# Optimization experiments

Hardware: AMD Instinct MI355X
Metric: run time of the kernel (lower is better)

Reference implementation:

```python
import jax, jax.numpy as jnp
import numpy as np

B, T, C, F = 8, 8, 1024, 4
N = T * C  # 8192 neurons
GUMBEL_KEY = 42  # fixed key standing in for torch's gumbel noise


def setup_inputs() -> dict:
    key = jax.random.key(0)
    kx, kw = jax.random.split(key)
    x = jax.random.normal(kx, (B * N, F), dtype=jnp.float32)
    # stacked ParameterList: weights[t] has shape [B, C, C]
    weights = jax.random.normal(kw, (T, B, C, C), dtype=jnp.float32)
    # cell type of each neuron; equal group sizes (1024 per type), interleaved
    cell_type_indices = (jnp.arange(N) % T).astype(jnp.int32)
    return {"x": x, "weights": weights, "cell_type_indices": cell_type_indices}


def reference(x, weights, cell_type_indices):
    n_types, bsz, cnt, _ = weights.shape
    nf = x.shape[-1]
    xr = x.reshape(bsz, -1, nf)  # [B, N, F]
    # per-type neuron indices, ascending within each type (pandas .index order);
    # stable argsort over types groups them contiguously -> [T, C]
    idx = jnp.argsort(cell_type_indices, stable=True).reshape(n_types, cnt)
    # gumbel_softmax(logits, tau=1, dim=1): softmax over the row axis (axis=2 here)
    g = jax.random.gumbel(jax.random.key(GUMBEL_KEY), weights.shape, weights.dtype)
    soft = jax.nn.softmax(weights + g, axis=2)  # [T, B, C, C]
    gathered = xr[:, idx]  # [B, T, C, F] per-group gather
    # grouped weighted matmul: out[t] = soft[t] @ gathered[:, t]
    res = jnp.einsum('tbij,btjf->btif', soft, gathered)  # [B, T, C, F]
    out = jnp.zeros_like(xr).at[:, idx].set(res)  # scatter back
    return out.reshape(-1, nf)
```

## Files before the change

### kernel.cpp

```cpp
#include <hip/hip_runtime.h>
#include <hip/hip_bf16.h>
#include <stdint.h>


__device__ __forceinline__ uint32_t rotl32(uint32_t x, uint32_t r) {
  return (x << r) | (x >> (32u - r));
}

__device__ __forceinline__ void threefry2x32(uint32_t c0, uint32_t c1,
                                             uint32_t& o0, uint32_t& o1) {
  const uint32_t k0 = 0u, k1 = 42u, k2 = 0x1BD11BDAu ^ 0u ^ 42u;
  uint32_t x0 = c0 + k0;
  uint32_t x1 = c1 + k1;
#define TF_R(r) { x0 += x1; x1 = rotl32(x1, r); x1 ^= x0; }
  TF_R(13) TF_R(15) TF_R(26) TF_R(6)
  x0 += k1; x1 += k2 + 1u;
  TF_R(17) TF_R(29) TF_R(16) TF_R(24)
  x0 += k2; x1 += k0 + 2u;
  TF_R(13) TF_R(15) TF_R(26) TF_R(6)
  x0 += k0; x1 += k1 + 3u;
  TF_R(17) TF_R(29) TF_R(16) TF_R(24)
  x0 += k1; x1 += k2 + 4u;
  TF_R(13) TF_R(15) TF_R(26) TF_R(6)
  x0 += k2; x1 += k0 + 5u;
#undef TF_R
  o0 = x0; o1 = x1;
}

__device__ __forceinline__ float gumbel_of(uint32_t e) {
  uint32_t o0, o1;
  threefry2x32(0u, e, o0, o1);
  uint32_t bits = o0 ^ o1;
  float f = __uint_as_float((bits >> 9) | 0x3f800000u) - 1.0f;
  f = fmaxf(f, 1.1754943508222875e-38f);
  return -__logf(-__logf(f));
}

template <int MODE>
__global__ __launch_bounds__(256) void pass1_kernel(
    const float* __restrict__ w, float* __restrict__ s, void* __restrict__ pout) {
  const int blk = blockIdx.x;
  const int ic  = blk & 63;
  const int tb  = blk >> 6;
  const int tid = threadIdx.x;
  const int i0  = ic * 16;

  const float4* w4 = (const float4*)w;
  const int base = tb * (1024 * 256) + i0 * 256 + tid;
  const uint32_t e_base = ((uint32_t)tb * 1024u + (uint32_t)i0) * 1024u + 4u * tid;

  float s0 = 0.f, s1 = 0.f, s2 = 0.f, s3 = 0.f;
  for (int r = 0; r < 16; ++r) {
    float4 wv = w4[base + r * 256];
    uint32_t e = e_base + (uint32_t)r * 1024u;
    float p0 = __expf(wv.x + gumbel_of(e + 0u));
    float p1 = __expf(wv.y + gumbel_of(e + 1u));
    float p2 = __expf(wv.z + gumbel_of(e + 2u));
    float p3 = __expf(wv.w + gumbel_of(e + 3u));
    s0 += p0; s1 += p1; s2 += p2; s3 += p3;
    if (MODE == 0) {
      ((float4*)pout)[base + r * 256] = make_float4(p0, p1, p2, p3);
    } else if (MODE == 1) {
      uint32_t b0 = (uint32_t)__bfloat16_as_ushort(__float2bfloat16(p0));
      uint32_t b1 = (uint32_t)__bfloat16_as_ushort(__float2bfloat16(p1));
      uint32_t b2 = (uint32_t)__bfloat16_as_ushort(__float2bfloat16(p2));
      uint32_t b3 = (uint32_t)__bfloat16_as_ushort(__float2bfloat16(p3));
      uint2 pk = make_uint2(b0 | (b1 << 16), b2 | (b3 << 16));
      ((uint2*)pout)[base + r * 256] = pk;
    }
  }
  float* sp = s + tb * 1024 + 4 * tid;
  atomicAdd(sp + 0, s0);
  atomicAdd(sp + 1, s1);
  atomicAdd(sp + 2, s2);
  atomicAdd(sp + 3, s3);
}

__device__ __forceinline__ void stage_y(const float* __restrict__ x,
                                        const float* __restrict__ s,
                                        int tb, int t, int b, int tid,
                                        float4* ylds) {
  const float4* x4 = (const float4*)x;
  for (int q = 0; q < 4; ++q) {
    int j = tid + 256 * q;
    float4 xv = x4[b * 8192 + t + 8 * j];
    float inv = 1.0f / s[tb * 1024 + j];
    int slot = (j & ~7) | ((j + (j >> 3)) & 7);
    ylds[slot] = make_float4(xv.x * inv, xv.y * inv, xv.z * inv, xv.w * inv);
  }
}

__device__ __forceinline__ void reduce_store(float a0, float a1, float a2, float a3,
                                             int lane, int b, int t, int i,
                                             float* __restrict__ out) {
#pragma unroll
  for (int mask = 32; mask >= 1; mask >>= 1) {
    a0 += __shfl_xor(a0, mask, 64);
    a1 += __shfl_xor(a1, mask, 64);
    a2 += __shfl_xor(a2, mask, 64);
    a3 += __shfl_xor(a3, mask, 64);
  }
  if (lane == 0) {
    ((float4*)out)[b * 8192 + t + 8 * i] = make_float4(a0, a1, a2, a3);
  }
}

__global__ __launch_bounds__(256) void pass2f_kernel(
    const float* __restrict__ p, const float* __restrict__ x,
    const float* __restrict__ s, float* __restrict__ out) {
  __shared__ float4 ylds[1024];
  const int blk = blockIdx.x;
  const int ig  = blk & 63;
  const int tb  = blk >> 6;
  const int t   = tb >> 3;
  const int b   = tb & 7;
  const int tid = threadIdx.x;

  stage_y(x, s, tb, t, b, tid, ylds);
  __syncthreads();

  const int wave = tid >> 6;
  const int lane = tid & 63;
  const float4* p4 = (const float4*)p;

  for (int rr = 0; rr < 4; ++rr) {
    const int i = ig * 16 + wave * 4 + rr;
    const int wbase = (tb * 1024 + i) * 256;
    float a0 = 0.f, a1 = 0.f, a2 = 0.f, a3 = 0.f;
#pragma unroll
    for (int m = 0; m < 4; ++m) {
      float4 pv = p4[wbase + lane + 64 * m];
      int jb = 4 * lane + 256 * m;
      float pr[4] = {pv.x, pv.y, pv.z, pv.w};
#pragma unroll
      for (int r = 0; r < 4; ++r) {
        int j = jb + r;
        int slot = (j & ~7) | ((j + (j >> 3)) & 7);
        float4 yv = ylds[slot];
        a0 = fmaf(pr[r], yv.x, a0);
        a1 = fmaf(pr[r], yv.y, a1);
        a2 = fmaf(pr[r], yv.z, a2);
        a3 = fmaf(pr[r], yv.w, a3);
      }
    }
    reduce_store(a0, a1, a2, a3, lane, b, t, i, out);
  }
}

__global__ __launch_bounds__(256) void pass2h_kernel(
    const uint2* __restrict__ p, const float* __restrict__ x,
    const float* __restrict__ s, float* __restrict__ out) {
  __shared__ float4 ylds[1024];
  const int blk = blockIdx.x;
  const int ig  = blk & 63;
  const int tb  = blk >> 6;
  const int t   = tb >> 3;
  const int b   = tb & 7;
  const int tid = threadIdx.x;

  stage_y(x, s, tb, t, b, tid, ylds);
  __syncthreads();

  const int wave = tid >> 6;
  const int lane = tid & 63;

  for (int rr = 0; rr < 4; ++rr) {
    const int i = ig * 16 + wave * 4 + rr;
    const int wbase = (tb * 1024 + i) * 256;
    float a0 = 0.f, a1 = 0.f, a2 = 0.f, a3 = 0.f;
#pragma unroll
    for (int m = 0; m < 4; ++m) {
      uint2 pk = p[wbase + lane + 64 * m];
      int jb = 4 * lane + 256 * m;
      float pr[4];
      pr[0] = __uint_as_float((pk.x & 0xFFFFu) << 16);
      pr[1] = __uint_as_float(pk.x & 0xFFFF0000u);
      pr[2] = __uint_as_float((pk.y & 0xFFFFu) << 16);
      pr[3] = __uint_as_float(pk.y & 0xFFFF0000u);
#pragma unroll
      for (int r = 0; r < 4; ++r) {
        int j = jb + r;
        int slot = (j & ~7) | ((j + (j >> 3)) & 7);
        float4 yv = ylds[slot];
        a0 = fmaf(pr[r], yv.x, a0);
        a1 = fmaf(pr[r], yv.y, a1);
        a2 = fmaf(pr[r], yv.z, a2);
        a3 = fmaf(pr[r], yv.w, a3);
      }
    }
    reduce_store(a0, a1, a2, a3, lane, b, t, i, out);
  }
}

__global__ __launch_bounds__(256) void pass2r_kernel(
    const float* __restrict__ w, const float* __restrict__ x,
    const float* __restrict__ s, float* __restrict__ out) {
  __shared__ float4 ylds[1024];
  const int blk = blockIdx.x;
  const int ig  = blk & 63;
  const int tb  = blk >> 6;
  const int t   = tb >> 3;
  const int b   = tb & 7;
  const int tid = threadIdx.x;

  stage_y(x, s, tb, t, b, tid, ylds);
  __syncthreads();

  const int wave = tid >> 6;
  const int lane = tid & 63;
  const float4* w4 = (const float4*)w;

  for (int rr = 0; rr < 4; ++rr) {
    const int i = ig * 16 + wave * 4 + rr;
    const uint32_t rb = (uint32_t)tb * 1024u + (uint32_t)i;
    const int wbase = (int)rb * 256;
    const uint32_t ebase = rb * 1024u;
    float a0 = 0.f, a1 = 0.f, a2 = 0.f, a3 = 0.f;
#pragma unroll
    for (int m = 0; m < 4; ++m) {
      float4 wv = w4[wbase + lane + 64 * m];
      int jb = 4 * lane + 256 * m;
      float wr[4] = {wv.x, wv.y, wv.z, wv.w};
#pragma unroll
      for (int r = 0; r < 4; ++r) {
        int j = jb + r;
        float pp = __expf(wr[r] + gumbel_of(ebase + (uint32_t)j));
        int slot = (j & ~7) | ((j + (j >> 3)) & 7);
        float4 yv = ylds[slot];
        a0 = fmaf(pp, yv.x, a0);
        a1 = fmaf(pp, yv.y, a1);
        a2 = fmaf(pp, yv.z, a2);
        a3 = fmaf(pp, yv.w, a3);
      }
    }
    reduce_store(a0, a1, a2, a3, lane, b, t, i, out);
  }
}

extern "C" void kernel_launch(void* const* d_in, const int* in_sizes, int n_in,
                              void* d_out, int out_size, void* d_ws, size_t ws_size,
                              hipStream_t stream) {
  const float* x = (const float*)d_in[0];
  const float* w = (const float*)d_in[1];
  float* out = (float*)d_out;

  float* s = (float*)d_ws;
  void*  p = (void*)((char*)d_ws + 64 * 1024 * sizeof(float));
  const size_t NP = 64ull * 1024 * 1024;
  const size_t need_f = 64 * 1024 * sizeof(float) + NP * 4;
  const size_t need_h = 64 * 1024 * sizeof(float) + NP * 2;

  hipMemsetAsync(s, 0, 64 * 1024 * sizeof(float), stream);
  if (ws_size >= need_f) {
    pass1_kernel<0><<<4096, 256, 0, stream>>>(w, s, p);
    pass2f_kernel<<<4096, 256, 0, stream>>>((const float*)p, x, s, out);
  } else if (ws_size >= need_h) {
    pass1_kernel<1><<<4096, 256, 0, stream>>>(w, s, p);
    pass2h_kernel<<<4096, 256, 0, stream>>>((const uint2*)p, x, s, out);
  } else {
    pass1_kernel<2><<<4096, 256, 0, stream>>>(w, s, nullptr);
    pass2r_kernel<<<4096, 256, 0, stream>>>(w, x, s, out);
  }
}
```

Before: 522.1 us.

## Store softmax numerators as bf16 and simplify gumbel-exp math

Drops the fp32 intermediate path, so whenever the workspace allows, the softmax numerators are written as bf16. This halves the intermediate write and read traffic between the two passes. It also rewrites exp(w + gumbel) as exp2(w*log2e) / (-log u) using hardware log/exp/rcp intrinsics, which removes one log and the composite exp. In exchange the intermediate loses precision, and the algebraic rewrite may shift numerics or overflow differently.

```diff
diff --git a/kernel.cpp b/kernel.cpp
--- a/kernel.cpp
+++ b/kernel.cpp
@@ -27,13 +27,17 @@
   o0 = x0; o1 = x1;
 }
 
-__device__ __forceinline__ float gumbel_of(uint32_t e) {
+#define LOG2E 1.442695040888963f
+#define NLN2 -0.6931471805599453f
+
+__device__ __forceinline__ float p_of(float w, uint32_t e) {
   uint32_t o0, o1;
   threefry2x32(0u, e, o0, o1);
   uint32_t bits = o0 ^ o1;
   float f = __uint_as_float((bits >> 9) | 0x3f800000u) - 1.0f;
   f = fmaxf(f, 1.1754943508222875e-38f);
-  return -__logf(-__logf(f));
+  float d = NLN2 * __builtin_amdgcn_logf(f);
+  return __builtin_amdgcn_exp2f(w * LOG2E) * __builtin_amdgcn_rcpf(d);
 }
 
 template <int MODE>
@@ -53,20 +57,17 @@
   for (int r = 0; r < 16; ++r) {
     float4 wv = w4[base + r * 256];
     uint32_t e = e_base + (uint32_t)r * 1024u;
-    float p0 = __expf(wv.x + gumbel_of(e + 0u));
-    float p1 = __expf(wv.y + gumbel_of(e + 1u));
-    float p2 = __expf(wv.z + gumbel_of(e + 2u));
-    float p3 = __expf(wv.w + gumbel_of(e + 3u));
+    float p0 = p_of(wv.x, e + 0u);
+    float p1 = p_of(wv.y, e + 1u);
+    float p2 = p_of(wv.z, e + 2u);
+    float p3 = p_of(wv.w, e + 3u);
     s0 += p0; s1 += p1; s2 += p2; s3 += p3;
-    if (MODE == 0) {
-      ((float4*)pout)[base + r * 256] = make_float4(p0, p1, p2, p3);
-    } else if (MODE == 1) {
+    if (MODE == 1) {
       uint32_t b0 = (uint32_t)__bfloat16_as_ushort(__float2bfloat16(p0));
       uint32_t b1 = (uint32_t)__bfloat16_as_ushort(__float2bfloat16(p1));
       uint32_t b2 = (uint32_t)__bfloat16_as_ushort(__float2bfloat16(p2));
       uint32_t b3 = (uint32_t)__bfloat16_as_ushort(__float2bfloat16(p3));
-      uint2 pk = make_uint2(b0 | (b1 << 16), b2 | (b3 << 16));
-      ((uint2*)pout)[base + r * 256] = pk;
+      ((uint2*)pout)[base + r * 256] = make_uint2(b0 | (b1 << 16), b2 | (b3 << 16));
     }
   }
   float* sp = s + tb * 1024 + 4 * tid;
@@ -105,8 +106,8 @@
   }
 }
 
-__global__ __launch_bounds__(256) void pass2f_kernel(
-    const float* __restrict__ p, const float* __restrict__ x,
+__global__ __launch_bounds__(256) void pass2h_kernel(
+    const uint2* __restrict__ p, const float* __restrict__ x,
     const float* __restrict__ s, float* __restrict__ out) {
   __shared__ float4 ylds[1024];
   const int blk = blockIdx.x;
@@ -121,7 +122,6 @@
 
   const int wave = tid >> 6;
   const int lane = tid & 63;
-  const float4* p4 = (const float4*)p;
 
   for (int rr = 0; rr < 4; ++rr) {
     const int i = ig * 16 + wave * 4 + rr;
@@ -129,9 +129,13 @@
     float a0 = 0.f, a1 = 0.f, a2 = 0.f, a3 = 0.f;
 #pragma unroll
     for (int m = 0; m < 4; ++m) {
-      float4 pv = p4[wbase + lane + 64 * m];
+      uint2 pk = p[wbase + lane + 64 * m];
       int jb = 4 * lane + 256 * m;
-      float pr[4] = {pv.x, pv.y, pv.z, pv.w};
+      float pr[4];
+      pr[0] = __uint_as_float((pk.x & 0xFFFFu) << 16);
+      pr[1] = __uint_as_float(pk.x & 0xFFFF0000u);
+      pr[2] = __uint_as_float((pk.y & 0xFFFFu) << 16);
+      pr[3] = __uint_as_float(pk.y & 0xFFFF0000u);
 #pragma unroll
       for (int r = 0; r < 4; ++r) {
         int j = jb + r;
@@ -147,51 +151,6 @@
   }
 }
 
-__global__ __launch_bounds__(256) void pass2h_kernel(
-    const uint2* __restrict__ p, const float* __restrict__ x,
-    const float* __restrict__ s, float* __restrict__ out) {
-  __shared__ float4 ylds[1024];
-  const int blk = blockIdx.x;
-  const int ig  = blk & 63;
-  const int tb  = blk >> 6;
-  const int t   = tb >> 3;
-  const int b   = tb & 7;
-  const int tid = threadIdx.x;
-
-  stage_y(x, s, tb, t, b, tid, ylds);
-  __syncthreads();
-
-  const int wave = tid >> 6;
-  const int lane = tid & 63;
-
-  for (int rr = 0; rr < 4; ++rr) {
-    const int i = ig * 16 + wave * 4 + rr;
-    const int wbase = (tb * 1024 + i) * 256;
-    float a0 = 0.f, a1 = 0.f, a2 = 0.f, a3 = 0.f;
-#pragma unroll
-    for (int m = 0; m < 4; ++m) {
-      uint2 pk = p[wbase + lane + 64 * m];
-      int jb = 4 * lane + 256 * m;
-      float pr[4];
-      pr[0] = __uint_as_float((pk.x & 0xFFFFu) << 16);
-      pr[1] = __uint_as_float(pk.x & 0xFFFF0000u);
-      pr[2] = __uint_as_float((pk.y & 0xFFFFu) << 16);
-      pr[3] = __uint_as_float(pk.y & 0xFFFF0000u);
-#pragma unroll
-      for (int r = 0; r < 4; ++r) {
-        int j = jb + r;
-        int slot = (j & ~7) | ((j + (j >> 3)) & 7);
-        float4 yv = ylds[slot];
-        a0 = fmaf(pr[r], yv.x, a0);
-        a1 = fmaf(pr[r], yv.y, a1);
-        a2 = fmaf(pr[r], yv.z, a2);
-        a3 = fmaf(pr[r], yv.w, a3);
-      }
-    }
-    reduce_store(a0, a1, a2, a3, lane, b, t, i, out);
-  }
-}
-
 __global__ __launch_bounds__(256) void pass2r_kernel(
     const float* __restrict__ w, const float* __restrict__ x,
     const float* __restrict__ s, float* __restrict__ out) {
@@ -224,7 +183,7 @@
 #pragma unroll
       for (int r = 0; r < 4; ++r) {
         int j = jb + r;
-        float pp = __expf(wr[r] + gumbel_of(ebase + (uint32_t)j));
+        float pp = p_of(wr[r], ebase + (uint32_t)j);
         int slot = (j & ~7) | ((j + (j >> 3)) & 7);
         float4 yv = ylds[slot];
         a0 = fmaf(pp, yv.x, a0);
@@ -247,14 +206,10 @@
   float* s = (float*)d_ws;
   void*  p = (void*)((char*)d_ws + 64 * 1024 * sizeof(float));
   const size_t NP = 64ull * 1024 * 1024;
-  const size_t need_f = 64 * 1024 * sizeof(float) + NP * 4;
   const size_t need_h = 64 * 1024 * sizeof(float) + NP * 2;
 
   hipMemsetAsync(s, 0, 64 * 1024 * sizeof(float), stream);
-  if (ws_size >= need_f) {
-    pass1_kernel<0><<<4096, 256, 0, stream>>>(w, s, p);
-    pass2f_kernel<<<4096, 256, 0, stream>>>((const float*)p, x, s, out);
-  } else if (ws_size >= need_h) {
+  if (ws_size >= need_h) {
     pass1_kernel<1><<<4096, 256, 0, stream>>>(w, s, p);
     pass2h_kernel<<<4096, 256, 0, stream>>>((const uint2*)p, x, s, out);
   } else {
```

Measured after the change: 475.0 us. 1.1x faster.
